# Kernel optimization log

Measured on AMD Instinct MI355X. Metric: run time of the kernel, lower is better.

Reference implementation:

```python
import jax, jax.numpy as jnp
import numpy as np

DIM = 4096
HEAD_DIM = 512
ROPE_DIM = 64
NOPE_DIM = HEAD_DIM - ROPE_DIM  # 448
RATIO = 4
COFF = 2  # overlap since ratio == 4
EPS = 1e-6
NEG = -1e30
COMPRESS_ROPE_THETA = 40000.0


def _hadamard(n):
    H = np.array([[1.0]], dtype=np.float32)
    while H.shape[0] < n:
        H = np.block([[H, H], [H, -H]])
    return (H / np.sqrt(n)).astype(np.float32)

H_MAT = jnp.asarray(_hadamard(HEAD_DIM))  # [512, 512], orthonormal Hadamard


def setup_inputs() -> dict:
    key = jax.random.key(0)
    ks = jax.random.split(key, 5)
    b, s = 4, 4096
    x = jax.random.normal(ks[0], (b, s, DIM), dtype=jnp.float32)
    W_kv = jax.random.normal(ks[1], (COFF * HEAD_DIM, DIM), dtype=jnp.float32) * 0.02
    W_gate = jax.random.normal(ks[2], (COFF * HEAD_DIM, DIM), dtype=jnp.float32) * 0.02
    ape = jax.random.normal(ks[3], (RATIO, COFF * HEAD_DIM), dtype=jnp.float32) * 0.02
    norm_w = jnp.ones((HEAD_DIM,), dtype=jnp.float32)
    # rotary table over compressed-block positions
    nb = s // RATIO
    inv_freq = 1.0 / (COMPRESS_ROPE_THETA ** (jnp.arange(0, ROPE_DIM, 2, dtype=jnp.float32) / ROPE_DIM))
    ang = jnp.arange(nb, dtype=jnp.float32)[:, None] * inv_freq[None, :]  # [nb, 32]
    freqs_cis = jnp.stack([jnp.cos(ang), jnp.sin(ang)], axis=-1)  # [nb, 32, 2]
    return {"x": x, "W_kv": W_kv, "W_gate": W_gate, "ape": ape,
            "norm_w": norm_w, "freqs_cis": freqs_cis, "start_pos": 0}


def _overlap_transform(t, fill):
    # t: [b, nb, RATIO, 2*d] -> [b, nb, 2*RATIO, d]
    b, nb, r, dd = t.shape
    d = dd // 2
    prev_first = jnp.concatenate(
        [jnp.full((b, 1, r, d), fill, t.dtype), t[:, :-1, :, :d]], axis=1)
    return jnp.concatenate([prev_first, t[..., d:]], axis=2)


def reference(x, W_kv, W_gate, ape, norm_w, freqs_cis, start_pos):
    b, s, _ = x.shape
    nb = s // RATIO
    # block-wise projections with absolute-within-block positional bias
    kv = jnp.einsum('bsd,od->bso', x, W_kv).reshape(b, nb, RATIO, COFF * HEAD_DIM) + ape
    score = jnp.einsum('bsd,od->bso', x, W_gate).reshape(b, nb, RATIO, COFF * HEAD_DIM)
    # overlap with previous block: [b, nb, 2*RATIO, HEAD_DIM]
    kv_w = _overlap_transform(kv, 0.0)
    sc_w = _overlap_transform(score, NEG)
    # channelwise softmax-gated pooling over the 2*RATIO window
    w = jax.nn.softmax(sc_w, axis=2)
    pooled = jnp.sum(w * kv_w, axis=2)  # [b, nb, HEAD_DIM]
    # RMSNorm
    var = jnp.mean(jnp.square(pooled), axis=-1, keepdims=True)
    pooled = norm_w * (pooled * jax.lax.rsqrt(var + EPS))
    # rotary on the rope slice
    nope, rope = pooled[..., :NOPE_DIM], pooled[..., NOPE_DIM:]
    rp = rope.reshape(b, nb, ROPE_DIM // 2, 2)
    xr, xi = rp[..., 0], rp[..., 1]
    fr, fi = freqs_cis[None, :, :, 0], freqs_cis[None, :, :, 1]
    rot = jnp.stack([xr * fr - xi * fi, xr * fi + xi * fr], axis=-1).reshape(b, nb, ROPE_DIM)
    out = jnp.concatenate([nope, rot], axis=-1)  # [b, nb, HEAD_DIM]
    # Hadamard rotation (rotate_activation)
    out = out @ H_MAT
    return out
```

## Files before the change

kernel.cpp:

```cpp
#include <hip/hip_runtime.h>
#include <hip/hip_bf16.h>
#include <stdint.h>

#define M_ROWS 16384
#define N_COLS 2048
#define K_DIM  4096
#define NEGV   -1e30f

typedef __bf16 bfv8 __attribute__((ext_vector_type(8)));
typedef float  f32x4 __attribute__((ext_vector_type(4)));
typedef unsigned short u16;

static __device__ __forceinline__ u16 f32_to_bf16_rne(float f) {
  union { float f; unsigned int u; } v; v.f = f;
  unsigned int u = v.u;
  u += 0x7fffu + ((u >> 16) & 1u);
  return (u16)(u >> 16);
}

__global__ __launch_bounds__(256) void k_cvt_x(const float* __restrict__ in,
                                               u16* __restrict__ out, long n) {
  long i = (long)blockIdx.x * blockDim.x + threadIdx.x;
  long base = i * 8;
  if (base >= n) return;
  float4 a = *(const float4*)(in + base);
  float4 b = *(const float4*)(in + base + 4);
  union { u16 s[8]; uint4 v; } o;
  o.s[0] = f32_to_bf16_rne(a.x); o.s[1] = f32_to_bf16_rne(a.y);
  o.s[2] = f32_to_bf16_rne(a.z); o.s[3] = f32_to_bf16_rne(a.w);
  o.s[4] = f32_to_bf16_rne(b.x); o.s[5] = f32_to_bf16_rne(b.y);
  o.s[6] = f32_to_bf16_rne(b.z); o.s[7] = f32_to_bf16_rne(b.w);
  *(uint4*)(out + base) = o.v;
}

__global__ __launch_bounds__(256) void k_cvt_w(const float* __restrict__ wkv,
                                               const float* __restrict__ wg,
                                               u16* __restrict__ out) {
  long i = (long)blockIdx.x * blockDim.x + threadIdx.x;
  long base = i * 8;
  const float* src = (base < 4194304L) ? (wkv + base) : (wg + (base - 4194304L));
  float4 a = *(const float4*)(src);
  float4 b = *(const float4*)(src + 4);
  union { u16 s[8]; uint4 v; } o;
  o.s[0] = f32_to_bf16_rne(a.x); o.s[1] = f32_to_bf16_rne(a.y);
  o.s[2] = f32_to_bf16_rne(a.z); o.s[3] = f32_to_bf16_rne(a.w);
  o.s[4] = f32_to_bf16_rne(b.x); o.s[5] = f32_to_bf16_rne(b.y);
  o.s[6] = f32_to_bf16_rne(b.z); o.s[7] = f32_to_bf16_rne(b.w);
  *(uint4*)(out + base) = o.v;
}

#define GLD16(g, l) __builtin_amdgcn_global_load_lds( \
    (const __attribute__((address_space(1))) unsigned int*)(g), \
    (__attribute__((address_space(3))) unsigned int*)(l), 16, 0, 0)

#define SB0 __builtin_amdgcn_sched_barrier(0)
#define BAR __builtin_amdgcn_s_barrier()
#define VM4 asm volatile("s_waitcnt vmcnt(4)" ::: "memory")

__global__ __launch_bounds__(512, 2) void k_gemm(const u16* __restrict__ A,
                                                 const u16* __restrict__ B,
                                                 float* __restrict__ C) {
  __shared__ u16 lds[65536];

  const int tid  = threadIdx.x;
  const int wid  = tid >> 6;
  const int lane = tid & 63;
  const int wr = wid >> 2, wc = wid & 3;
  const int fr = lane & 15, fq = lane >> 4;

  int o = blockIdx.x;
  int swz = (o & 7) * 64 + (o >> 3);
  const int bm = swz >> 3, bn = swz & 7;
  const int gm0 = bm << 8, gn0 = bn << 8;

  int aoff[8], boff[4];
#pragma unroll
  for (int mi = 0; mi < 8; ++mi) {
    int row = (wr << 7) + (mi << 4) + fr;
    int Gp = (((row & 1) << 2) | fq) ^ ((row >> 1) & 7);
    aoff[mi] = (row >> 1) * 64 + Gp * 8;
  }
#pragma unroll
  for (int ni = 0; ni < 4; ++ni) {
    int row = (wc << 6) + (ni << 4) + fr;
    int Gp = (((row & 1) << 2) | fq) ^ ((row >> 1) & 7);
    boff[ni] = (row >> 1) * 64 + Gp * 8;
  }

  const int s0 = tid, s1 = 512 + tid;
  const int l0 = s0 >> 3, G0 = (s0 & 7) ^ (l0 & 7);
  const int r0 = 2 * l0 + (G0 >> 2), g0 = (G0 & 3) << 3;
  const int l1 = s1 >> 3, G1 = (s1 & 7) ^ (l1 & 7);
  const int r1 = 2 * l1 + (G1 >> 2), g1 = (G1 & 3) << 3;
  const u16* pA0 = A + ((size_t)(gm0 + r0) << 12) + g0;
  const u16* pA1 = A + ((size_t)(gm0 + r1) << 12) + g1;
  const u16* pB0 = B + ((size_t)(gn0 + r0) << 12) + g0;
  const u16* pB1 = B + ((size_t)(gn0 + r1) << 12) + g1;
  const int du0 = wid << 9;
  const int du1 = 4096 + (wid << 9);

#define STAGE_A(Q, KK, KTN) do { \
  GLD16(pA0 + (KTN) + (KK) * 32, &lds[(Q) * 16384 + (KK) * 8192 + du0]); \
  GLD16(pA1 + (KTN) + (KK) * 32, &lds[(Q) * 16384 + (KK) * 8192 + du1]); } while (0)
#define STAGE_B(Q, KK, KTN) do { \
  GLD16(pB0 + (KTN) + (KK) * 32, &lds[32768 + (Q) * 16384 + (KK) * 8192 + du0]); \
  GLD16(pB1 + (KTN) + (KK) * 32, &lds[32768 + (Q) * 16384 + (KK) * 8192 + du1]); } while (0)
#define LDA(P, KK, MI) (*(const bfv8*)&lds[(P) * 16384 + (KK) * 8192 + aoff[MI]])
#define LDB(P, KK, NI) (*(const bfv8*)&lds[32768 + (P) * 16384 + (KK) * 8192 + boff[NI]])
#define MF(AV, BV, MI, NI) acc[MI][NI] = __builtin_amdgcn_mfma_f32_16x16x32_bf16(AV, BV, acc[MI][NI], 0, 0, 0)
#define MF4(AV, MI) do { MF(AV, b0, MI, 0); MF(AV, b1, MI, 1); MF(AV, b2, MI, 2); MF(AV, b3, MI, 3); } while (0)

  f32x4 acc[8][4];
#pragma unroll
  for (int i = 0; i < 8; ++i)
#pragma unroll
    for (int j = 0; j < 4; ++j) acc[i][j] = (f32x4){0.f, 0.f, 0.f, 0.f};

  STAGE_A(0, 0, 0); STAGE_B(0, 0, 0); STAGE_A(0, 1, 0); STAGE_B(0, 1, 0);
  SB0; VM4; BAR; SB0;

  bfv8 a0, a1, a2, a3, a4, a5, a6, a7, b0, b1, b2, b3;

#define KTILE(P, Q, KTN) do { \
  a0 = LDA(P, 0, 0); a1 = LDA(P, 0, 1); a2 = LDA(P, 0, 2); a3 = LDA(P, 0, 3); \
  b0 = LDB(P, 0, 0); b1 = LDB(P, 0, 1); b2 = LDB(P, 0, 2); b3 = LDB(P, 0, 3); \
  STAGE_A(Q, 0, KTN); \
  SB0; BAR; SB0; \
  __builtin_amdgcn_s_setprio(1); \
  MF4(a0, 0); MF4(a1, 1); MF4(a2, 2); MF4(a3, 3); \
  __builtin_amdgcn_s_setprio(0); SB0; \
  a4 = LDA(P, 0, 4); a5 = LDA(P, 0, 5); a6 = LDA(P, 0, 6); a7 = LDA(P, 0, 7); \
  STAGE_B(Q, 0, KTN); \
  SB0; VM4; BAR; SB0; \
  __builtin_amdgcn_s_setprio(1); \
  MF4(a4, 4); MF4(a5, 5); MF4(a6, 6); MF4(a7, 7); \
  __builtin_amdgcn_s_setprio(0); SB0; \
  a0 = LDA(P, 1, 0); a1 = LDA(P, 1, 1); a2 = LDA(P, 1, 2); a3 = LDA(P, 1, 3); \
  b0 = LDB(P, 1, 0); b1 = LDB(P, 1, 1); b2 = LDB(P, 1, 2); b3 = LDB(P, 1, 3); \
  STAGE_A(Q, 1, KTN); \
  SB0; BAR; SB0; \
  __builtin_amdgcn_s_setprio(1); \
  MF4(a0, 0); MF4(a1, 1); MF4(a2, 2); MF4(a3, 3); \
  __builtin_amdgcn_s_setprio(0); SB0; \
  a4 = LDA(P, 1, 4); a5 = LDA(P, 1, 5); a6 = LDA(P, 1, 6); a7 = LDA(P, 1, 7); \
  STAGE_B(Q, 1, KTN); \
  SB0; VM4; BAR; SB0; \
  __builtin_amdgcn_s_setprio(1); \
  MF4(a4, 4); MF4(a5, 5); MF4(a6, 6); MF4(a7, 7); \
  __builtin_amdgcn_s_setprio(0); SB0; \
} while (0)

  for (int i = 0; i < 32; ++i) {
    const int kt1 = (2 * i + 1) << 6;
    const int kt2 = (i == 31) ? 0 : (2 * i + 2) << 6;
    KTILE(0, 1, kt1);
    KTILE(1, 0, kt2);
  }

#pragma unroll
  for (int mi = 0; mi < 8; ++mi) {
    int row = gm0 + (wr << 7) + (mi << 4) + (fq << 2);
#pragma unroll
    for (int ni = 0; ni < 4; ++ni) {
      int col = gn0 + (wc << 6) + (ni << 4) + fr;
#pragma unroll
      for (int j = 0; j < 4; ++j)
        C[(size_t)(row + j) * N_COLS + col] = acc[mi][ni][j];
    }
  }
#undef KTILE
#undef STAGE_A
#undef STAGE_B
#undef LDA
#undef LDB
#undef MF
#undef MF4
}

__global__ __launch_bounds__(256) void k_pool(const float* __restrict__ kvsc,
                                              const float* __restrict__ ape,
                                              const float* __restrict__ norm_w,
                                              const float* __restrict__ freqs,
                                              float* __restrict__ out) {
  __shared__ float sm[512];
  __shared__ float red[8];
  const int tid = threadIdx.x;
  const int bid = blockIdx.x;
  const int b = bid >> 10, ib = bid & 1023;

  float ss = 0.f;
#pragma unroll
  for (int cc = 0; cc < 2; ++cc) {
    int c = tid + (cc << 8);
    float kvv[8], scv[8];
    if (ib > 0) {
      size_t mb = ((size_t)b * 4096 + (size_t)(ib - 1) * 4);
#pragma unroll
      for (int p = 0; p < 4; ++p) {
        size_t ro = (mb + p) * N_COLS;
        kvv[p] = kvsc[ro + c] + ape[p * 1024 + c];
        scv[p] = kvsc[ro + 1024 + c];
      }
    } else {
#pragma unroll
      for (int p = 0; p < 4; ++p) { kvv[p] = 0.f; scv[p] = NEGV; }
    }
    size_t mb2 = ((size_t)b * 4096 + (size_t)ib * 4);
#pragma unroll
    for (int r = 0; r < 4; ++r) {
      size_t ro = (mb2 + r) * N_COLS;
      kvv[4 + r] = kvsc[ro + 512 + c] + ape[r * 1024 + 512 + c];
      scv[4 + r] = kvsc[ro + 1024 + 512 + c];
    }
    float mx = scv[0];
#pragma unroll
    for (int p = 1; p < 8; ++p) mx = fmaxf(mx, scv[p]);
    float se = 0.f, ac = 0.f;
#pragma unroll
    for (int p = 0; p < 8; ++p) {
      float e = __expf(scv[p] - mx);
      se += e; ac += e * kvv[p];
    }
    float pooled = ac / se;
    sm[c] = pooled;
    ss += pooled * pooled;
  }
#pragma unroll
  for (int m = 1; m < 64; m <<= 1) ss += __shfl_xor(ss, m, 64);
  if ((tid & 63) == 0) red[tid >> 6] = ss;
  __syncthreads();
  float sumsq = red[0] + red[1] + red[2] + red[3];
  float scale = rsqrtf(sumsq * (1.f / 512.f) + 1e-6f);
  sm[tid]       = sm[tid]       * scale * norm_w[tid];
  sm[tid + 256] = sm[tid + 256] * scale * norm_w[tid + 256];
  __syncthreads();
  if (tid < 32) {
    int j = tid;
    float xr = sm[448 + 2 * j], xi = sm[449 + 2 * j];
    float fr = freqs[((size_t)ib * 32 + j) * 2];
    float fi = freqs[((size_t)ib * 32 + j) * 2 + 1];
    sm[448 + 2 * j] = xr * fr - xi * fi;
    sm[449 + 2 * j] = xr * fi + xi * fr;
  }
  __syncthreads();
#pragma unroll
  for (int k = 0; k < 9; ++k) {
    int low = tid & ((1 << k) - 1);
    int i0 = ((tid >> k) << (k + 1)) | low;
    int i1 = i0 | (1 << k);
    float a = sm[i0], bb = sm[i1];
    sm[i0] = a + bb; sm[i1] = a - bb;
    __syncthreads();
  }
  const float OSC = 0.044194173824159216f;
  size_t ob = (size_t)bid * 512;
  out[ob + tid]       = sm[tid] * OSC;
  out[ob + tid + 256] = sm[tid + 256] * OSC;
}

extern "C" void kernel_launch(void* const* d_in, const int* in_sizes, int n_in,
                              void* d_out, int out_size, void* d_ws, size_t ws_size,
                              hipStream_t stream) {
  const float* x      = (const float*)d_in[0];
  const float* W_kv   = (const float*)d_in[1];
  const float* W_gate = (const float*)d_in[2];
  const float* ape    = (const float*)d_in[3];
  const float* norm_w = (const float*)d_in[4];
  const float* freqs  = (const float*)d_in[5];
  float* out = (float*)d_out;

  char* ws = (char*)d_ws;
  u16*   xb   = (u16*)ws;
  u16*   wb   = (u16*)(ws + 134217728L);
  float* kvsc = (float*)(ws + 134217728L + 16777216L);

  hipLaunchKernelGGL(k_cvt_x, dim3(32768), dim3(256), 0, stream, x, xb, (long)67108864L);
  hipLaunchKernelGGL(k_cvt_w, dim3(4096), dim3(256), 0, stream, W_kv, W_gate, wb);
  hipLaunchKernelGGL(k_gemm, dim3(512), dim3(512), 0, stream, xb, wb, kvsc);
  hipLaunchKernelGGL(k_pool, dim3(4096), dim3(256), 0, stream, kvsc, ape, norm_w, freqs, out);
}
```

Measured before the change: 333.4 us.

## Fuse x fp32-to-bf16 conversion into GEMM A-tile loads; store bf16 intermediates

Drops the separate x conversion kernel. The GEMM now loads fp32 x tiles straight into registers, packs them to bf16 and writes them to swizzled LDS, instead of using direct global-to-LDS copies of a pre-converted buffer. The GEMM output is also stored as bf16 and the pooling kernel widens it back to float, which halves intermediate traffic but loses some precision. The A path now goes through VGPRs and needs full vmcnt(0) and lgkmcnt(0) waits, and each GEMM block reads twice as many A bytes, which may reduce overlap.

```diff
diff --git a/kernel.cpp b/kernel.cpp
--- a/kernel.cpp
+++ b/kernel.cpp
@@ -18,19 +18,18 @@
   return (u16)(u >> 16);
 }
 
-__global__ __launch_bounds__(256) void k_cvt_x(const float* __restrict__ in,
-                                               u16* __restrict__ out, long n) {
-  long i = (long)blockIdx.x * blockDim.x + threadIdx.x;
-  long base = i * 8;
-  if (base >= n) return;
-  float4 a = *(const float4*)(in + base);
-  float4 b = *(const float4*)(in + base + 4);
-  union { u16 s[8]; uint4 v; } o;
-  o.s[0] = f32_to_bf16_rne(a.x); o.s[1] = f32_to_bf16_rne(a.y);
-  o.s[2] = f32_to_bf16_rne(a.z); o.s[3] = f32_to_bf16_rne(a.w);
-  o.s[4] = f32_to_bf16_rne(b.x); o.s[5] = f32_to_bf16_rne(b.y);
-  o.s[6] = f32_to_bf16_rne(b.z); o.s[7] = f32_to_bf16_rne(b.w);
-  *(uint4*)(out + base) = o.v;
+static __device__ __forceinline__ float b2f(u16 b) {
+  union { unsigned int u; float f; } v; v.u = ((unsigned int)b) << 16;
+  return v.f;
+}
+
+static __device__ __forceinline__ uint4 pack8(float4 a, float4 b) {
+  union { __hip_bfloat162 h[4]; uint4 v; } o;
+  o.h[0] = __float22bfloat162_rn(make_float2(a.x, a.y));
+  o.h[1] = __float22bfloat162_rn(make_float2(a.z, a.w));
+  o.h[2] = __float22bfloat162_rn(make_float2(b.x, b.y));
+  o.h[3] = __float22bfloat162_rn(make_float2(b.z, b.w));
+  return o.v;
 }
 
 __global__ __launch_bounds__(256) void k_cvt_w(const float* __restrict__ wkv,
@@ -55,11 +54,12 @@
 
 #define SB0 __builtin_amdgcn_sched_barrier(0)
 #define BAR __builtin_amdgcn_s_barrier()
-#define VM4 asm volatile("s_waitcnt vmcnt(4)" ::: "memory")
-
-__global__ __launch_bounds__(512, 2) void k_gemm(const u16* __restrict__ A,
+#define VM0 asm volatile("s_waitcnt vmcnt(0)" ::: "memory")
+#define LGK0 asm volatile("s_waitcnt lgkmcnt(0)" ::: "memory")
+
+__global__ __launch_bounds__(512, 2) void k_gemm(const float* __restrict__ A,
                                                  const u16* __restrict__ B,
-                                                 float* __restrict__ C) {
+                                                 u16* __restrict__ C) {
   __shared__ u16 lds[65536];
 
   const int tid  = threadIdx.x;
@@ -92,19 +92,36 @@
   const int r0 = 2 * l0 + (G0 >> 2), g0 = (G0 & 3) << 3;
   const int l1 = s1 >> 3, G1 = (s1 & 7) ^ (l1 & 7);
   const int r1 = 2 * l1 + (G1 >> 2), g1 = (G1 & 3) << 3;
-  const u16* pA0 = A + ((size_t)(gm0 + r0) << 12) + g0;
-  const u16* pA1 = A + ((size_t)(gm0 + r1) << 12) + g1;
   const u16* pB0 = B + ((size_t)(gn0 + r0) << 12) + g0;
   const u16* pB1 = B + ((size_t)(gn0 + r1) << 12) + g1;
   const int du0 = wid << 9;
   const int du1 = 4096 + (wid << 9);
 
-#define STAGE_A(Q, KK, KTN) do { \
-  GLD16(pA0 + (KTN) + (KK) * 32, &lds[(Q) * 16384 + (KK) * 8192 + du0]); \
-  GLD16(pA1 + (KTN) + (KK) * 32, &lds[(Q) * 16384 + (KK) * 8192 + du1]); } while (0)
+  const int ar = tid & 255;
+  const int ah = tid >> 8;
+  const float* pAf = A + ((size_t)(gm0 + ar) << 12) + (ah << 5);
+  const int al = ar >> 1;
+  const int ahbase = ah << 13;
+  int awoff[4];
+#pragma unroll
+  for (int g = 0; g < 4; ++g) {
+    int Gp = (((ar & 1) << 2) | g) ^ (al & 7);
+    awoff[g] = ahbase + al * 64 + Gp * 8;
+  }
+
 #define STAGE_B(Q, KK, KTN) do { \
   GLD16(pB0 + (KTN) + (KK) * 32, &lds[32768 + (Q) * 16384 + (KK) * 8192 + du0]); \
   GLD16(pB1 + (KTN) + (KK) * 32, &lds[32768 + (Q) * 16384 + (KK) * 8192 + du1]); } while (0)
+#define LOADA(KTN) do { \
+  fA0 = *(const float4*)(pAf + (KTN));      fA1 = *(const float4*)(pAf + (KTN) + 4);  \
+  fA2 = *(const float4*)(pAf + (KTN) + 8);  fA3 = *(const float4*)(pAf + (KTN) + 12); \
+  fA4 = *(const float4*)(pAf + (KTN) + 16); fA5 = *(const float4*)(pAf + (KTN) + 20); \
+  fA6 = *(const float4*)(pAf + (KTN) + 24); fA7 = *(const float4*)(pAf + (KTN) + 28); } while (0)
+#define WRITEA(Q) do { \
+  *(uint4*)&lds[(Q) * 16384 + awoff[0]] = pack8(fA0, fA1); \
+  *(uint4*)&lds[(Q) * 16384 + awoff[1]] = pack8(fA2, fA3); \
+  *(uint4*)&lds[(Q) * 16384 + awoff[2]] = pack8(fA4, fA5); \
+  *(uint4*)&lds[(Q) * 16384 + awoff[3]] = pack8(fA6, fA7); } while (0)
 #define LDA(P, KK, MI) (*(const bfv8*)&lds[(P) * 16384 + (KK) * 8192 + aoff[MI]])
 #define LDB(P, KK, NI) (*(const bfv8*)&lds[32768 + (P) * 16384 + (KK) * 8192 + boff[NI]])
 #define MF(AV, BV, MI, NI) acc[MI][NI] = __builtin_amdgcn_mfma_f32_16x16x32_bf16(AV, BV, acc[MI][NI], 0, 0, 0)
@@ -116,35 +133,41 @@
 #pragma unroll
     for (int j = 0; j < 4; ++j) acc[i][j] = (f32x4){0.f, 0.f, 0.f, 0.f};
 
-  STAGE_A(0, 0, 0); STAGE_B(0, 0, 0); STAGE_A(0, 1, 0); STAGE_B(0, 1, 0);
-  SB0; VM4; BAR; SB0;
+  float4 fA0, fA1, fA2, fA3, fA4, fA5, fA6, fA7;
+
+  LOADA(0);
+  STAGE_B(0, 0, 0); STAGE_B(0, 1, 0);
+  WRITEA(0);
+  VM0; LGK0;
+  SB0; BAR; SB0;
 
   bfv8 a0, a1, a2, a3, a4, a5, a6, a7, b0, b1, b2, b3;
 
 #define KTILE(P, Q, KTN) do { \
   a0 = LDA(P, 0, 0); a1 = LDA(P, 0, 1); a2 = LDA(P, 0, 2); a3 = LDA(P, 0, 3); \
   b0 = LDB(P, 0, 0); b1 = LDB(P, 0, 1); b2 = LDB(P, 0, 2); b3 = LDB(P, 0, 3); \
-  STAGE_A(Q, 0, KTN); \
+  LOADA(KTN); \
   SB0; BAR; SB0; \
   __builtin_amdgcn_s_setprio(1); \
   MF4(a0, 0); MF4(a1, 1); MF4(a2, 2); MF4(a3, 3); \
   __builtin_amdgcn_s_setprio(0); SB0; \
   a4 = LDA(P, 0, 4); a5 = LDA(P, 0, 5); a6 = LDA(P, 0, 6); a7 = LDA(P, 0, 7); \
-  STAGE_B(Q, 0, KTN); \
-  SB0; VM4; BAR; SB0; \
+  STAGE_B(Q, 0, KTN); STAGE_B(Q, 1, KTN); \
+  SB0; BAR; SB0; \
   __builtin_amdgcn_s_setprio(1); \
   MF4(a4, 4); MF4(a5, 5); MF4(a6, 6); MF4(a7, 7); \
   __builtin_amdgcn_s_setprio(0); SB0; \
   a0 = LDA(P, 1, 0); a1 = LDA(P, 1, 1); a2 = LDA(P, 1, 2); a3 = LDA(P, 1, 3); \
   b0 = LDB(P, 1, 0); b1 = LDB(P, 1, 1); b2 = LDB(P, 1, 2); b3 = LDB(P, 1, 3); \
-  STAGE_A(Q, 1, KTN); \
+  WRITEA(Q); \
+  LGK0; \
   SB0; BAR; SB0; \
   __builtin_amdgcn_s_setprio(1); \
   MF4(a0, 0); MF4(a1, 1); MF4(a2, 2); MF4(a3, 3); \
   __builtin_amdgcn_s_setprio(0); SB0; \
   a4 = LDA(P, 1, 4); a5 = LDA(P, 1, 5); a6 = LDA(P, 1, 6); a7 = LDA(P, 1, 7); \
-  STAGE_B(Q, 1, KTN); \
-  SB0; VM4; BAR; SB0; \
+  VM0; \
+  SB0; BAR; SB0; \
   __builtin_amdgcn_s_setprio(1); \
   MF4(a4, 4); MF4(a5, 5); MF4(a6, 6); MF4(a7, 7); \
   __builtin_amdgcn_s_setprio(0); SB0; \
@@ -165,19 +188,20 @@
       int col = gn0 + (wc << 6) + (ni << 4) + fr;
 #pragma unroll
       for (int j = 0; j < 4; ++j)
-        C[(size_t)(row + j) * N_COLS + col] = acc[mi][ni][j];
+        C[(size_t)(row + j) * N_COLS + col] = f32_to_bf16_rne(acc[mi][ni][j]);
     }
   }
 #undef KTILE
-#undef STAGE_A
 #undef STAGE_B
+#undef LOADA
+#undef WRITEA
 #undef LDA
 #undef LDB
 #undef MF
 #undef MF4
 }
 
-__global__ __launch_bounds__(256) void k_pool(const float* __restrict__ kvsc,
+__global__ __launch_bounds__(256) void k_pool(const u16* __restrict__ kvsc,
                                               const float* __restrict__ ape,
                                               const float* __restrict__ norm_w,
                                               const float* __restrict__ freqs,
@@ -198,8 +222,8 @@
 #pragma unroll
       for (int p = 0; p < 4; ++p) {
         size_t ro = (mb + p) * N_COLS;
-        kvv[p] = kvsc[ro + c] + ape[p * 1024 + c];
-        scv[p] = kvsc[ro + 1024 + c];
+        kvv[p] = b2f(kvsc[ro + c]) + ape[p * 1024 + c];
+        scv[p] = b2f(kvsc[ro + 1024 + c]);
       }
     } else {
 #pragma unroll
@@ -209,8 +233,8 @@
 #pragma unroll
     for (int r = 0; r < 4; ++r) {
       size_t ro = (mb2 + r) * N_COLS;
-      kvv[4 + r] = kvsc[ro + 512 + c] + ape[r * 1024 + 512 + c];
-      scv[4 + r] = kvsc[ro + 1024 + 512 + c];
+      kvv[4 + r] = b2f(kvsc[ro + 512 + c]) + ape[r * 1024 + 512 + c];
+      scv[4 + r] = b2f(kvsc[ro + 1024 + 512 + c]);
     }
     float mx = scv[0];
 #pragma unroll
@@ -270,12 +294,10 @@
   float* out = (float*)d_out;
 
   char* ws = (char*)d_ws;
-  u16*   xb   = (u16*)ws;
-  u16*   wb   = (u16*)(ws + 134217728L);
-  float* kvsc = (float*)(ws + 134217728L + 16777216L);
-
-  hipLaunchKernelGGL(k_cvt_x, dim3(32768), dim3(256), 0, stream, x, xb, (long)67108864L);
+  u16* wb   = (u16*)ws;
+  u16* kvsc = (u16*)(ws + 16777216L);
+
   hipLaunchKernelGGL(k_cvt_w, dim3(4096), dim3(256), 0, stream, W_kv, W_gate, wb);
-  hipLaunchKernelGGL(k_gemm, dim3(512), dim3(512), 0, stream, xb, wb, kvsc);
+  hipLaunchKernelGGL(k_gemm, dim3(512), dim3(512), 0, stream, x, wb, kvsc);
   hipLaunchKernelGGL(k_pool, dim3(4096), dim3(256), 0, stream, kvsc, ape, norm_w, freqs, out);
 }
```

After: 536.2 us. 60.9% more time.
